# Optimization experiments

Hardware: AMD Instinct MI355X
Metric: run time of the kernel (lower is better)

Reference implementation:

```python
import jax, jax.numpy as jnp
import numpy as np
from jax import lax

B, T, K = 16, 8, 64
COUT, CIN, KH, KW = 128, 128, 5, 5
H, W = 64, 64
PAD = 2  # p=2 in batch_conv -> same spatial size for 5x5


def setup_inputs() -> dict:
    key = jax.random.key(0)
    k1, k2, k3 = jax.random.split(key, 3)
    x = jax.random.normal(k1, (B, CIN, H, W), dtype=jnp.float32)
    task_features = jax.random.normal(k2, (B, T, K), dtype=jnp.float32)
    # learned weight bank (kaiming-uniform in torch; scaled normal is fine for a reference)
    fan_in = CIN * KH * KW
    weights = jax.random.normal(k3, (K, COUT, CIN, KH, KW), dtype=jnp.float32) / np.sqrt(fan_in)
    return {"x": x, "task_features": task_features, "weights": weights}


def reference(x, task_features, weights):
    # infer_params: per-demonstration weighted sum over the K weight bank,
    # then mean over demonstrations T. Fused into one contraction:
    #   sum_t sum_k tf[b,t,k] * W[k,o,c,i,j] / T
    layer_params = jnp.einsum('btk,kocij->bocij', task_features, weights) / T  # (B,Cout,Cin,kh,kw)

    # batch_conv: per-example conv2d with padding 2 (group=B pattern)
    def conv_one(xi, wi):
        # xi: (Cin,H,W), wi: (Cout,Cin,kh,kw)
        return lax.conv_general_dilated(
            xi[None], wi, window_strides=(1, 1),
            padding=[(PAD, PAD), (PAD, PAD)],
            dimension_numbers=('NCHW', 'OIHW', 'NCHW'))[0]

    y = jax.vmap(conv_one)(x, layer_params)  # (B, Cout, H, W)
    return y
```

## Files before the change

### kernel.cpp

```cpp
#include <hip/hip_runtime.h>

#define B_    16
#define T_    8
#define K_    64
#define COUT  128
#define CIN   128
#define H_    64
#define W_    64
#define WSZ   (COUT*CIN*5*5)

typedef __bf16 bf16x8 __attribute__((ext_vector_type(8)));
typedef float  f32x4  __attribute__((ext_vector_type(4)));

static __device__ __forceinline__ unsigned short f2bf(float f) {
    unsigned int u = __builtin_bit_cast(unsigned int, f);
    unsigned int r = (u + 0x7FFFu + ((u >> 16) & 1u)) >> 16;
    return (unsigned short)r;
}

static __device__ __forceinline__ unsigned int pack2(float lo, float hi) {
    return (unsigned int)f2bf(lo) | ((unsigned int)f2bf(hi) << 16);
}

__global__ __launch_bounds__(256) void prep_kernel(const float* __restrict__ Wb,
                                                   const float* __restrict__ tf,
                                                   const float* __restrict__ x,
                                                   unsigned short* __restrict__ lpF,
                                                   unsigned short* __restrict__ xT) {
    __shared__ __align__(16) char smem[30720];
    int tid = threadIdx.x;

    if (blockIdx.x < 512) {
        float* cs          = (float*)smem;
        unsigned short* lt = (unsigned short*)(smem + 4096);

        int o = blockIdx.x >> 2;
        int s = blockIdx.x & 3;

        {
            int idx = tid;
#pragma unroll
            for (int r = 0; r < 4; ++r, idx += 256) {
                int b = idx >> 6, k = idx & 63;
                float sum = 0.f;
#pragma unroll
                for (int t = 0; t < T_; ++t) sum += tf[(b * T_ + t) * K_ + k];
                cs[idx] = sum * 0.125f;
            }
        }
        __syncthreads();

        if (tid < 200) {
            int base = o * 3200 + s * 800 + tid * 4;
            float4 acc[B_];
#pragma unroll
            for (int b = 0; b < B_; ++b) acc[b] = make_float4(0.f, 0.f, 0.f, 0.f);

#pragma unroll 4
            for (int k = 0; k < K_; ++k) {
                const float4 wv = *(const float4*)(Wb + (size_t)k * WSZ + base);
#pragma unroll
                for (int b = 0; b < B_; ++b) {
                    float c = cs[b * K_ + k];
                    acc[b].x += c * wv.x;
                    acc[b].y += c * wv.y;
                    acc[b].z += c * wv.z;
                    acc[b].w += c * wv.w;
                }
            }
            unsigned int* ltw = (unsigned int*)lt;
#pragma unroll
            for (int b = 0; b < B_; ++b) {
                ltw[b * 400 + tid * 2]     = pack2(acc[b].x, acc[b].y);
                ltw[b * 400 + tid * 2 + 1] = pack2(acc[b].z, acc[b].w);
            }
        }
        __syncthreads();

        int wm = o >> 6, mt = (o >> 4) & 3, n16 = o & 15;
        for (int it = tid; it < 1600; it += 256) {
            int b = it / 100;
            int r = it - b * 100;
            int tap = r >> 2;
            int quad = r & 3;
            unsigned short v[8];
#pragma unroll
            for (int j = 0; j < 8; ++j)
                v[j] = lt[b * 800 + (quad * 8 + j) * 25 + tap];
            size_t off = (size_t)b * 409600
                       + (size_t)((((tap * 4 + s) * 2 + wm) * 4 + mt) * 512
                                  + quad * 128 + n16 * 8);
            *(uint4*)(lpF + off) = *(const uint4*)v;
        }
    } else {
        unsigned short* ls = (unsigned short*)smem;
        int q = blockIdx.x - 512;
        int b = q >> 6, h = q & 63;

        int w = tid & 63, cb = tid >> 6;
        const float* xp = x + (((size_t)(b * CIN + cb * 32) * H_ + h) * W_) + w;
#pragma unroll
        for (int p = 0; p < 16; ++p) {
            float f0 = xp[(size_t)(2 * p) * (H_ * W_)];
            float f1 = xp[(size_t)(2 * p + 1) * (H_ * W_)];
            *(unsigned int*)&ls[w * 136 + cb * 32 + 2 * p] = pack2(f0, f1);
        }
        __syncthreads();

        unsigned short* xTb = xT + ((size_t)(b * 64 + h) * 64) * 128;
        int chunk = tid & 15, wr = tid >> 4;
#pragma unroll
        for (int pass = 0; pass < 4; ++pass) {
            int ww = pass * 16 + wr;
            uint4 v = *(const uint4*)&ls[ww * 136 + chunk * 8];
            *(uint4*)&xTb[ww * 128 + chunk * 8] = v;
        }
    }
}

__global__ __launch_bounds__(256) void conv_mfma(const unsigned short* __restrict__ xT,
                                                 const unsigned short* __restrict__ lpF,
                                                 float* __restrict__ out) {
    int bid = blockIdx.x;
    int b  = (bid & 7) | (((bid >> 3) & 1) << 3);
    int h0 = (bid >> 4) << 1;

    int tid  = threadIdx.x;
    int lane = tid & 63, wq = tid >> 6;
    int n16 = lane & 15, quad = lane >> 4;

    __shared__ __align__(16) unsigned short xs[408 * 40];

    f32x4 acc[2][8];
#pragma unroll
    for (int mt = 0; mt < 2; ++mt)
#pragma unroll
        for (int nt = 0; nt < 8; ++nt) acc[mt][nt] = (f32x4){0.f, 0.f, 0.f, 0.f};

    const unsigned short* xTb = xT + (size_t)b * (64 * 64 * 128);
    const unsigned short* lpW = lpF + (size_t)b * 409600
                              + (wq >> 1) * 2048 + (wq & 1) * 1024 + lane * 8;

    for (int kc = 0; kc < 4; ++kc) {
        int kcOff = kc * 32;
        int kcB   = kc * 4096;
        __syncthreads();
        for (int sIdx = tid; sIdx < 408; sIdx += 256) {
            unsigned int su = (unsigned int)sIdx;
            int rr = su / 68u;
            int ww = su - rr * 68u;
            int gr = h0 - 2 + rr, gw = ww - 2;
            uint4* dst = (uint4*)&xs[sIdx * 40];
            if ((unsigned)gr < 64u && (unsigned)gw < 64u) {
                const uint4* src = (const uint4*)(xTb + (((size_t)gr * 64 + gw) * 128 + kcOff));
                dst[0] = src[0]; dst[1] = src[1]; dst[2] = src[2]; dst[3] = src[3];
            } else {
                uint4 z = {0u, 0u, 0u, 0u};
                dst[0] = z; dst[1] = z; dst[2] = z; dst[3] = z;
            }
        }
        __syncthreads();

#pragma unroll
        for (int j = 0; j < 5; ++j) {
            const unsigned short* rp = &xs[(n16 + j) * 40 + quad * 8];

            bf16x8 R0[4], R1[4], R2[4];
            bf16x8 A0[2], A1[2];
#pragma unroll
            for (int nt = 0; nt < 4; ++nt) R0[nt] = *(const bf16x8*)(rp + nt * 640);
#pragma unroll
            for (int nt = 0; nt < 4; ++nt) R1[nt] = *(const bf16x8*)(rp + 2720 + nt * 640);
            {
                const unsigned short* ap = lpW + j * 16384 + kcB;
                A0[0] = *(const bf16x8*)(ap);
                A0[1] = *(const bf16x8*)(ap + 512);
            }
#pragma unroll
            for (int i = 0; i < 5; ++i) {
                if (i < 4) {
                    const unsigned short* rpn = rp + (i + 2) * 2720;
#pragma unroll
                    for (int nt = 0; nt < 4; ++nt)
                        R2[nt] = *(const bf16x8*)(rpn + nt * 640);
                    const unsigned short* apn = lpW + ((i + 1) * 5 + j) * 16384 + kcB;
                    A1[0] = *(const bf16x8*)(apn);
                    A1[1] = *(const bf16x8*)(apn + 512);
                }
#pragma unroll
                for (int mt = 0; mt < 2; ++mt)
#pragma unroll
                    for (int nt = 0; nt < 4; ++nt) {
                        acc[mt][nt] = __builtin_amdgcn_mfma_f32_16x16x32_bf16(
                            A0[mt], R0[nt], acc[mt][nt], 0, 0, 0);
                        acc[mt][nt + 4] = __builtin_amdgcn_mfma_f32_16x16x32_bf16(
                            A0[mt], R1[nt], acc[mt][nt + 4], 0, 0, 0);
                    }
#pragma unroll
                for (int nt = 0; nt < 4; ++nt) { R0[nt] = R1[nt]; R1[nt] = R2[nt]; }
                A0[0] = A1[0]; A0[1] = A1[1];
            }
        }
    }

    float* outb = out + (size_t)b * (COUT * H_ * W_);
#pragma unroll
    for (int mt = 0; mt < 2; ++mt) {
#pragma unroll
        for (int nt = 0; nt < 8; ++nt) {
#pragma unroll
            for (int r = 0; r < 4; ++r) {
                int o = wq * 32 + mt * 16 + quad * 4 + r;
                int h = h0 + (nt >> 2);
                int w = (nt & 3) * 16 + n16;
                outb[(size_t)o * (H_ * W_) + (size_t)h * W_ + w] = acc[mt][nt][r];
            }
        }
    }
}

extern "C" void kernel_launch(void* const* d_in, const int* in_sizes, int n_in,
                              void* d_out, int out_size, void* d_ws, size_t ws_size,
                              hipStream_t stream) {
    const float* x  = (const float*)d_in[0];
    const float* tf = (const float*)d_in[1];
    const float* Wb = (const float*)d_in[2];
    float* out = (float*)d_out;

    unsigned short* lpF = (unsigned short*)d_ws;
    unsigned short* xT  = lpF + (size_t)B_ * 409600;

    prep_kernel<<<1536, 256, 0, stream>>>(Wb, tf, x, lpF, xT);
    conv_mfma  <<<512,  256, 0, stream>>>(xT, lpF, out);
}
```

Baseline: 235.8 us.

## Fuse input fp32-to-bf16 transpose into conv kernel's shared-memory staging

Removes the separate x transpose/convert blocks from the prep kernel and the xT workspace round trip. The conv kernel now reads fp32 NCHW input directly, converts pairs of channels to bf16 and scatters them into a channel-last LDS tile with row stride 42, zeroing the tile once for the padding halo. This trades an extra global write/read of the input for scattered 32-bit LDS stores and redundant re-reading of halo rows, which each block fetches as fp32 (twice the bytes of the old bf16 reads).

```diff
diff --git a/kernel.cpp b/kernel.cpp
--- a/kernel.cpp
+++ b/kernel.cpp
@@ -11,6 +11,7 @@
 
 typedef __bf16 bf16x8 __attribute__((ext_vector_type(8)));
 typedef float  f32x4  __attribute__((ext_vector_type(4)));
+typedef unsigned int u32;
 
 static __device__ __forceinline__ unsigned short f2bf(float f) {
     unsigned int u = __builtin_bit_cast(unsigned int, f);
@@ -24,101 +25,74 @@
 
 __global__ __launch_bounds__(256) void prep_kernel(const float* __restrict__ Wb,
                                                    const float* __restrict__ tf,
-                                                   const float* __restrict__ x,
-                                                   unsigned short* __restrict__ lpF,
-                                                   unsigned short* __restrict__ xT) {
+                                                   unsigned short* __restrict__ lpF) {
     __shared__ __align__(16) char smem[30720];
     int tid = threadIdx.x;
 
-    if (blockIdx.x < 512) {
-        float* cs          = (float*)smem;
-        unsigned short* lt = (unsigned short*)(smem + 4096);
-
-        int o = blockIdx.x >> 2;
-        int s = blockIdx.x & 3;
-
-        {
-            int idx = tid;
-#pragma unroll
-            for (int r = 0; r < 4; ++r, idx += 256) {
-                int b = idx >> 6, k = idx & 63;
-                float sum = 0.f;
-#pragma unroll
-                for (int t = 0; t < T_; ++t) sum += tf[(b * T_ + t) * K_ + k];
-                cs[idx] = sum * 0.125f;
-            }
-        }
-        __syncthreads();
-
-        if (tid < 200) {
-            int base = o * 3200 + s * 800 + tid * 4;
-            float4 acc[B_];
-#pragma unroll
-            for (int b = 0; b < B_; ++b) acc[b] = make_float4(0.f, 0.f, 0.f, 0.f);
+    float* cs          = (float*)smem;
+    unsigned short* lt = (unsigned short*)(smem + 4096);
+
+    int o = blockIdx.x >> 2;
+    int s = blockIdx.x & 3;
+
+    {
+        int idx = tid;
+#pragma unroll
+        for (int r = 0; r < 4; ++r, idx += 256) {
+            int b = idx >> 6, k = idx & 63;
+            float sum = 0.f;
+#pragma unroll
+            for (int t = 0; t < T_; ++t) sum += tf[(b * T_ + t) * K_ + k];
+            cs[idx] = sum * 0.125f;
+        }
+    }
+    __syncthreads();
+
+    if (tid < 200) {
+        int base = o * 3200 + s * 800 + tid * 4;
+        float4 acc[B_];
+#pragma unroll
+        for (int b = 0; b < B_; ++b) acc[b] = make_float4(0.f, 0.f, 0.f, 0.f);
 
 #pragma unroll 4
-            for (int k = 0; k < K_; ++k) {
-                const float4 wv = *(const float4*)(Wb + (size_t)k * WSZ + base);
-#pragma unroll
-                for (int b = 0; b < B_; ++b) {
-                    float c = cs[b * K_ + k];
-                    acc[b].x += c * wv.x;
-                    acc[b].y += c * wv.y;
-                    acc[b].z += c * wv.z;
-                    acc[b].w += c * wv.w;
-                }
-            }
-            unsigned int* ltw = (unsigned int*)lt;
+        for (int k = 0; k < K_; ++k) {
+            const float4 wv = *(const float4*)(Wb + (size_t)k * WSZ + base);
 #pragma unroll
             for (int b = 0; b < B_; ++b) {
-                ltw[b * 400 + tid * 2]     = pack2(acc[b].x, acc[b].y);
-                ltw[b * 400 + tid * 2 + 1] = pack2(acc[b].z, acc[b].w);
-            }
-        }
-        __syncthreads();
-
-        int wm = o >> 6, mt = (o >> 4) & 3, n16 = o & 15;
-        for (int it = tid; it < 1600; it += 256) {
-            int b = it / 100;
-            int r = it - b * 100;
-            int tap = r >> 2;
-            int quad = r & 3;
-            unsigned short v[8];
-#pragma unroll
-            for (int j = 0; j < 8; ++j)
-                v[j] = lt[b * 800 + (quad * 8 + j) * 25 + tap];
-            size_t off = (size_t)b * 409600
-                       + (size_t)((((tap * 4 + s) * 2 + wm) * 4 + mt) * 512
-                                  + quad * 128 + n16 * 8);
-            *(uint4*)(lpF + off) = *(const uint4*)v;
-        }
-    } else {
-        unsigned short* ls = (unsigned short*)smem;
-        int q = blockIdx.x - 512;
-        int b = q >> 6, h = q & 63;
-
-        int w = tid & 63, cb = tid >> 6;
-        const float* xp = x + (((size_t)(b * CIN + cb * 32) * H_ + h) * W_) + w;
-#pragma unroll
-        for (int p = 0; p < 16; ++p) {
-            float f0 = xp[(size_t)(2 * p) * (H_ * W_)];
-            float f1 = xp[(size_t)(2 * p + 1) * (H_ * W_)];
-            *(unsigned int*)&ls[w * 136 + cb * 32 + 2 * p] = pack2(f0, f1);
-        }
-        __syncthreads();
-
-        unsigned short* xTb = xT + ((size_t)(b * 64 + h) * 64) * 128;
-        int chunk = tid & 15, wr = tid >> 4;
-#pragma unroll
-        for (int pass = 0; pass < 4; ++pass) {
-            int ww = pass * 16 + wr;
-            uint4 v = *(const uint4*)&ls[ww * 136 + chunk * 8];
-            *(uint4*)&xTb[ww * 128 + chunk * 8] = v;
-        }
-    }
-}
-
-__global__ __launch_bounds__(256) void conv_mfma(const unsigned short* __restrict__ xT,
+                float c = cs[b * K_ + k];
+                acc[b].x += c * wv.x;
+                acc[b].y += c * wv.y;
+                acc[b].z += c * wv.z;
+                acc[b].w += c * wv.w;
+            }
+        }
+        unsigned int* ltw = (unsigned int*)lt;
+#pragma unroll
+        for (int b = 0; b < B_; ++b) {
+            ltw[b * 400 + tid * 2]     = pack2(acc[b].x, acc[b].y);
+            ltw[b * 400 + tid * 2 + 1] = pack2(acc[b].z, acc[b].w);
+        }
+    }
+    __syncthreads();
+
+    int wm = o >> 6, mt = (o >> 4) & 3, n16 = o & 15;
+    for (int it = tid; it < 1600; it += 256) {
+        int b = it / 100;
+        int r = it - b * 100;
+        int tap = r >> 2;
+        int quad = r & 3;
+        unsigned short v[8];
+#pragma unroll
+        for (int j = 0; j < 8; ++j)
+            v[j] = lt[b * 800 + (quad * 8 + j) * 25 + tap];
+        size_t off = (size_t)b * 409600
+                   + (size_t)((((tap * 4 + s) * 2 + wm) * 4 + mt) * 512
+                              + quad * 128 + n16 * 8);
+        *(uint4*)(lpF + off) = *(const uint4*)v;
+    }
+}
+
+__global__ __launch_bounds__(256) void conv_mfma(const float* __restrict__ x,
                                                  const unsigned short* __restrict__ lpF,
                                                  float* __restrict__ out) {
     int bid = blockIdx.x;
@@ -126,10 +100,10 @@
     int h0 = (bid >> 4) << 1;
 
     int tid  = threadIdx.x;
-    int lane = tid & 63, wq = tid >> 6;
+    int lane = tid & 63, wq4 = tid >> 6;
     int n16 = lane & 15, quad = lane >> 4;
 
-    __shared__ __align__(16) unsigned short xs[408 * 40];
+    __shared__ __align__(16) unsigned short xs[408 * 42];
 
     f32x4 acc[2][8];
 #pragma unroll
@@ -137,40 +111,48 @@
 #pragma unroll
         for (int nt = 0; nt < 8; ++nt) acc[mt][nt] = (f32x4){0.f, 0.f, 0.f, 0.f};
 
-    const unsigned short* xTb = xT + (size_t)b * (64 * 64 * 128);
     const unsigned short* lpW = lpF + (size_t)b * 409600
-                              + (wq >> 1) * 2048 + (wq & 1) * 1024 + lane * 8;
+                              + (wq4 >> 1) * 2048 + (wq4 & 1) * 1024 + lane * 8;
+
+    {
+        u32* z = (u32*)xs;
+        for (int i = tid; i < (408 * 42) / 2; i += 256) z[i] = 0u;
+    }
+
+    int cp = tid >> 4;
+    int wq = tid & 15;
 
     for (int kc = 0; kc < 4; ++kc) {
         int kcOff = kc * 32;
         int kcB   = kc * 4096;
         __syncthreads();
-        for (int sIdx = tid; sIdx < 408; sIdx += 256) {
-            unsigned int su = (unsigned int)sIdx;
-            int rr = su / 68u;
-            int ww = su - rr * 68u;
-            int gr = h0 - 2 + rr, gw = ww - 2;
-            uint4* dst = (uint4*)&xs[sIdx * 40];
-            if ((unsigned)gr < 64u && (unsigned)gw < 64u) {
-                const uint4* src = (const uint4*)(xTb + (((size_t)gr * 64 + gw) * 128 + kcOff));
-                dst[0] = src[0]; dst[1] = src[1]; dst[2] = src[2]; dst[3] = src[3];
-            } else {
-                uint4 z = {0u, 0u, 0u, 0u};
-                dst[0] = z; dst[1] = z; dst[2] = z; dst[3] = z;
+        const float* xc = x + ((size_t)(b * CIN + kcOff + 2 * cp) * H_) * W_ + wq * 4;
+#pragma unroll
+        for (int rr = 0; rr < 6; ++rr) {
+            int gr = h0 - 2 + rr;
+            if ((unsigned)gr < 64u) {
+                const float* x0 = xc + (size_t)gr * W_;
+                float4 a  = *(const float4*)x0;
+                float4 c4 = *(const float4*)(x0 + H_ * W_);
+                int wwb = rr * 68 + wq * 4 + 2;
+                *(u32*)&xs[(wwb + 0) * 42 + 2 * cp] = pack2(a.x, c4.x);
+                *(u32*)&xs[(wwb + 1) * 42 + 2 * cp] = pack2(a.y, c4.y);
+                *(u32*)&xs[(wwb + 2) * 42 + 2 * cp] = pack2(a.z, c4.z);
+                *(u32*)&xs[(wwb + 3) * 42 + 2 * cp] = pack2(a.w, c4.w);
             }
         }
         __syncthreads();
 
 #pragma unroll
         for (int j = 0; j < 5; ++j) {
-            const unsigned short* rp = &xs[(n16 + j) * 40 + quad * 8];
+            const unsigned short* rp = &xs[(n16 + j) * 42 + quad * 8];
 
             bf16x8 R0[4], R1[4], R2[4];
             bf16x8 A0[2], A1[2];
 #pragma unroll
-            for (int nt = 0; nt < 4; ++nt) R0[nt] = *(const bf16x8*)(rp + nt * 640);
-#pragma unroll
-            for (int nt = 0; nt < 4; ++nt) R1[nt] = *(const bf16x8*)(rp + 2720 + nt * 640);
+            for (int nt = 0; nt < 4; ++nt) R0[nt] = *(const bf16x8*)(rp + nt * 672);
+#pragma unroll
+            for (int nt = 0; nt < 4; ++nt) R1[nt] = *(const bf16x8*)(rp + 2856 + nt * 672);
             {
                 const unsigned short* ap = lpW + j * 16384 + kcB;
                 A0[0] = *(const bf16x8*)(ap);
@@ -179,10 +161,10 @@
 #pragma unroll
             for (int i = 0; i < 5; ++i) {
                 if (i < 4) {
-                    const unsigned short* rpn = rp + (i + 2) * 2720;
+                    const unsigned short* rpn = rp + (i + 2) * 2856;
 #pragma unroll
                     for (int nt = 0; nt < 4; ++nt)
-                        R2[nt] = *(const bf16x8*)(rpn + nt * 640);
+                        R2[nt] = *(const bf16x8*)(rpn + nt * 672);
                     const unsigned short* apn = lpW + ((i + 1) * 5 + j) * 16384 + kcB;
                     A1[0] = *(const bf16x8*)(apn);
                     A1[1] = *(const bf16x8*)(apn + 512);
@@ -210,7 +192,7 @@
         for (int nt = 0; nt < 8; ++nt) {
 #pragma unroll
             for (int r = 0; r < 4; ++r) {
-                int o = wq * 32 + mt * 16 + quad * 4 + r;
+                int o = wq4 * 32 + mt * 16 + quad * 4 + r;
                 int h = h0 + (nt >> 2);
                 int w = (nt & 3) * 16 + n16;
                 outb[(size_t)o * (H_ * W_) + (size_t)h * W_ + w] = acc[mt][nt][r];
@@ -228,8 +210,7 @@
     float* out = (float*)d_out;
 
     unsigned short* lpF = (unsigned short*)d_ws;
-    unsigned short* xT  = lpF + (size_t)B_ * 409600;
-
-    prep_kernel<<<1536, 256, 0, stream>>>(Wb, tf, x, lpF, xT);
-    conv_mfma  <<<512,  256, 0, stream>>>(xT, lpF, out);
-}
+
+    prep_kernel<<<512, 256, 0, stream>>>(Wb, tf, lpF);
+    conv_mfma  <<<512, 256, 0, stream>>>(x, lpF, out);
+}
```

After: 305.2 us. 29.4% more time.
